# Performance work log

Measured on AMD Instinct MI355X. Metric: run time of the kernel, lower is better.

The kernel has to match this reference:

```python
import jax, jax.numpy as jnp
import numpy as np
from jax import lax

EPS = 1e-9
DN = ('NCHW', 'OIHW', 'NCHW')


def _conv2d_valid(x, w):
    return lax.conv_general_dilated(x, w, window_strides=(1, 1), padding='VALID',
                                    dimension_numbers=DN)


def setup_inputs() -> dict:
    key = jax.random.key(0)
    kx, ky = jax.random.split(key)
    x = jax.random.normal(kx, (32, 64, 96, 96), dtype=jnp.float32)
    y = jax.random.normal(ky, (32, 64, 13, 13), dtype=jnp.float32)  # (K prototypes, C, kh, kw)
    return {'x': x, 'y': y}


def reference(x, y):
    # Per-prototype L2 normalization of y over (C, kh, kw)
    y_norm = jnp.clip(jnp.sqrt(jnp.sum(y * y, axis=(1, 2, 3), keepdims=True)), EPS)
    normed_y = y / y_norm
    # Sliding-window L2 norm of x. The torch code convolves x^2 with ones of
    # shape (K, C, kh, kw) producing K identical channels; we compute one
    # channel and broadcast (same math, less work).
    ones_k = jnp.ones((1,) + y.shape[1:], dtype=x.dtype)
    x_norm = jnp.clip(jnp.sqrt(_conv2d_valid(x * x, ones_k)), EPS)  # (B,1,H',W')
    diss = _conv2d_valid(x, normed_y) / x_norm  # (B,K,H',W')
    return jax.nn.relu(diss)
```

## Files before the change

kernel.cpp:

```cpp
#include <hip/hip_runtime.h>
#include <hip/hip_bf16.h>

#define B_   32
#define C_   64
#define H_   96
#define W_   96
#define K_   32
#define R_   13
#define HO_  84
#define WO_  84
#define HW_  (H_*W_)
#define OHW_ (HO_*WO_)
#define CRR_ (C_*R_*R_)
#define RR_  (R_*R_)

#define TILE_ 16
#define PW_   28
#define NPIX_ (PW_*PW_)
#define HBUF_ 12544
#define BUF_  (2*HBUF_)
#define LDS_NEW (2*BUF_)
#define REGB_ (NPIX_*16)
#define LDS_FB (2*REGB_)

#define XBF_BYTES  ((size_t)B_*4*HW_*32)
#define UG_BYTES   ((size_t)RR_*4096)
#define S_BYTES    ((size_t)B_*HW_*4)
#define INV_BYTES  ((size_t)B_*OHW_*4)
#define WS_NEED    (XBF_BYTES + UG_BYTES + S_BYTES + INV_BYTES)

typedef unsigned int u32;
typedef unsigned short u16;
typedef __attribute__((ext_vector_type(16))) float f32x16;
typedef __attribute__((ext_vector_type(4))) u32 u32x4;

static __device__ __forceinline__ u16 f2bf(float v){
    __hip_bfloat16 h = __float2bfloat16(v);
    return *reinterpret_cast<u16*>(&h);
}

#define MFMA(acc, a, b) asm("v_mfma_f32_32x32x16_bf16 %0, %1, %2, %0" \
                            : "+v"(acc) : "v"(a), "v"(b))

static __device__ __forceinline__ void gload_lds16(const void* g, void* l){
    __builtin_amdgcn_global_load_lds(
        (const __attribute__((address_space(1))) unsigned char*)g,
        (__attribute__((address_space(3))) unsigned char*)l, 16, 0, 0);
}

static __device__ void prep_y_block(const float* __restrict__ y,
                                    unsigned char* __restrict__ u_g,
                                    int k, int tid, float* red){
    const float* yk = y + (size_t)k * CRR_;
    float ss = 0.f;
    for (int idx = tid; idx < CRR_; idx += 256){ float v = yk[idx]; ss += v*v; }
    for (int off = 32; off; off >>= 1) ss += __shfl_down(ss, off);
    if ((tid & 63) == 0) red[tid >> 6] = ss;
    __syncthreads();
    float inv = 1.f / fmaxf(sqrtf(red[0]+red[1]+red[2]+red[3]), 1e-9f);

    int c = tid & 63, grp = tid >> 6;
    int inoff = (k << 5) | ((c & 15) << 1);
    for (int base = 0; base < RR_; base += 4){
        int ij = base + grp;
        if (ij < RR_){
            int i = ij / R_, jx = ij % R_;
            float v = yk[c*RR_ + ij] * inv;
            size_t slice = ((size_t)(c >> 4) * RR_ + jx*R_ + i) << 10;
            *(u16*)(u_g + slice + inoff) = f2bf(v);
        }
    }
}

__global__ void k_prep_y(const float* __restrict__ y, unsigned char* __restrict__ u_g){
    __shared__ float red[4];
    prep_y_block(y, u_g, blockIdx.x, threadIdx.x, red);
}

__global__ void k_prep(const float* __restrict__ x, const float* __restrict__ y,
                       float* __restrict__ s, unsigned char* __restrict__ xbf,
                       unsigned char* __restrict__ u_g){
    __shared__ float red[4];
    int bb = blockIdx.x;
    if (bb < K_){ prep_y_block(y, u_g, bb, threadIdx.x, red); return; }
    int idx = (bb - K_)*256 + threadIdx.x;
    int b = idx / HW_, r = idx % HW_;
    const float* xb = x + (size_t)b * C_ * HW_ + r;
    float acc = 0.f;
    #pragma unroll
    for (int q = 0; q < 4; ++q){
        int c0 = q*16;
        float a0 = xb[(size_t)(c0+0)*HW_],  a1 = xb[(size_t)(c0+1)*HW_];
        float a2 = xb[(size_t)(c0+2)*HW_],  a3 = xb[(size_t)(c0+3)*HW_];
        float a4 = xb[(size_t)(c0+4)*HW_],  a5 = xb[(size_t)(c0+5)*HW_];
        float a6 = xb[(size_t)(c0+6)*HW_],  a7 = xb[(size_t)(c0+7)*HW_];
        float a8 = xb[(size_t)(c0+8)*HW_],  a9 = xb[(size_t)(c0+9)*HW_];
        float aa = xb[(size_t)(c0+10)*HW_], ab = xb[(size_t)(c0+11)*HW_];
        float ac = xb[(size_t)(c0+12)*HW_], ad = xb[(size_t)(c0+13)*HW_];
        float ae = xb[(size_t)(c0+14)*HW_], af = xb[(size_t)(c0+15)*HW_];
        acc += a0*a0+a1*a1+a2*a2+a3*a3+a4*a4+a5*a5+a6*a6+a7*a7
             + a8*a8+a9*a9+aa*aa+ab*ab+ac*ac+ad*ad+ae*ae+af*af;
        u32x4 q0 = { f2bf(a0)|((u32)f2bf(a1)<<16), f2bf(a2)|((u32)f2bf(a3)<<16),
                     f2bf(a4)|((u32)f2bf(a5)<<16), f2bf(a6)|((u32)f2bf(a7)<<16) };
        u32x4 q1 = { f2bf(a8)|((u32)f2bf(a9)<<16), f2bf(aa)|((u32)f2bf(ab)<<16),
                     f2bf(ac)|((u32)f2bf(ad)<<16), f2bf(ae)|((u32)f2bf(af)<<16) };
        unsigned char* ob = xbf + ((size_t)(b*4 + q)*HW_ + r)*32;
        *(u32x4*)(ob)      = q0;
        *(u32x4*)(ob + 16) = q1;
    }
    s[idx] = acc;
}

__global__ void k_sq(const float* __restrict__ x, float* __restrict__ s){
    int idx = blockIdx.x*256 + threadIdx.x;
    int b = idx / HW_, r = idx % HW_;
    const float* xb = x + (size_t)b * C_ * HW_;
    float acc = 0.f;
    #pragma unroll
    for (int c = 0; c < C_; ++c){ float v = xb[(size_t)c*HW_ + r]; acc += v*v; }
    s[idx] = acc;
}

__global__ void k_inv(const float* __restrict__ s, float* __restrict__ inv_xn){
    int idx = blockIdx.x*256 + threadIdx.x;
    int b = idx / OHW_, r = idx % OHW_;
    int oh = r / WO_, ow = r % WO_;
    const float* sb = s + (size_t)b*HW_ + oh*W_ + ow;
    float acc = 0.f;
    for (int i = 0; i < R_; ++i){
        #pragma unroll
        for (int j = 0; j < R_; ++j) acc += sb[i*W_ + j];
    }
    inv_xn[idx] = 1.f / fmaxf(sqrtf(acc), 1e-9f);
}

__launch_bounds__(256, 3)
__global__ void k_main(const unsigned char* __restrict__ xbf,
                       const unsigned char* __restrict__ u_g,
                       const float* __restrict__ inv_xn, float* __restrict__ out){
    extern __shared__ unsigned char lds[];

    int bb0 = blockIdx.x;
    int bb  = (bb0 & 7) * 144 + (bb0 >> 3);
    int b  = bb / 36;
    int tt = bb % 36;
    int oy = (tt / 6) * TILE_;
    int ox = (tt % 6) * TILE_;

    int tid  = threadIdx.x;
    int lane = tid & 63;
    int wv   = tid >> 6;
    int ks   = lane >> 5;
    int rb   = (lane >> 4) & 1;
    int cx   = lane & 15;
    int kpr  = lane & 31;

    const unsigned char* xq = xbf + (size_t)b*4*HW_*32;
    int aoff = (kpr << 5) + (ks << 4);
    int pb   = (4*wv + rb) * PW_ + cx;

    int goff[13], loff[13];
    #pragma unroll
    for (int cb = 0; cb < 13; ++cb){
        int cs = cb*64; if (cs > NPIX_-64) cs = NPIX_-64;
        int p = cs + lane;
        int py = p / PW_, px = p % PW_;
        int gy = oy + py; if (gy > H_-1) gy = H_-1;
        int gx = ox + px; if (gx > W_-1) gx = W_-1;
        goff[cb] = (gy*W_ + gx) << 5;
        loff[cb] = cs << 4;
    }

#define STAGE(bufsel, q) {                                                   \
        const unsigned char* src = xq + (size_t)(q)*HW_*32;                  \
        unsigned char* dst = lds + (bufsel)*BUF_;                            \
        for (int t = wv; t < 26; t += 4){                                    \
            int h = t & 1, cb = t >> 1;                                      \
            gload_lds16(src + goff[cb] + h*16, dst + h*HBUF_ + loff[cb]);    \
        }                                                                    \
    }

    f32x16 acc0 = {}, acc1 = {};
    STAGE(0, 0);

    for (int pass = 0; pass < 4; ++pass){
        __syncthreads();
        if (pass < 3) STAGE((pass+1)&1, pass+1);

        const unsigned char* xh = lds + (pass&1)*BUF_ + ks*HBUF_;
        const unsigned char* ug = u_g + ((size_t)pass*RR_ << 10);

        u32x4 A0 = *(const u32x4*)(ug              + aoff);
        u32x4 A1 = *(const u32x4*)(ug + (1 << 10)  + aoff);
        u32x4 A2 = *(const u32x4*)(ug + (2 << 10)  + aoff);
        u32x4 A3 = *(const u32x4*)(ug + (3 << 10)  + aoff);

        const unsigned char* col0 = xh + pb*16;
        u32x4 d0 = *(const u32x4*)(col0);
        u32x4 d1 = *(const u32x4*)(col0 +   PW_*16);
        u32x4 d2 = *(const u32x4*)(col0 + 2*PW_*16);
        u32x4 d3 = *(const u32x4*)(col0 + 3*PW_*16);
        u32x4 d4 = *(const u32x4*)(col0 + 4*PW_*16);

        int t = 0;
        for (int jx = 0; jx < R_; ++jx){
            const unsigned char* col  = xh + (pb + jx)*16;
            const unsigned char* ncol = col + 16;
            u32x4 e0, e1, e2, e3, e4;
            bool more = (jx < R_-1);
            #pragma unroll
            for (int i = 0; i < R_; ++i, ++t){
                int tn = t + 4; if (tn > RR_-1) tn = RR_-1;
                u32x4 An = *(const u32x4*)(ug + ((size_t)tn << 10) + aoff);
                u32x4 dn = d4;
                if (i < 10) dn = *(const u32x4*)(col + (i+5)*PW_*16);
                if (more){
                    if (i == 8)  e0 = *(const u32x4*)(ncol);
                    if (i == 9)  e1 = *(const u32x4*)(ncol +   PW_*16);
                    if (i == 10) e2 = *(const u32x4*)(ncol + 2*PW_*16);
                    if (i == 11) e3 = *(const u32x4*)(ncol + 3*PW_*16);
                    if (i == 12) e4 = *(const u32x4*)(ncol + 4*PW_*16);
                }
                __builtin_amdgcn_s_setprio(1);
                MFMA(acc0, A0, d0);
                MFMA(acc1, A0, d2);
                __builtin_amdgcn_s_setprio(0);
                A0 = A1; A1 = A2; A2 = A3; A3 = An;
                d0 = d1; d1 = d2; d2 = d3; d3 = d4; d4 = dn;
            }
            if (more){ d0 = e0; d1 = e1; d2 = e2; d3 = e3; d4 = e4; }
        }
    }

    int ow = ox + cx;
#define EPI(ACC, F) {                                                        \
        int oh = oy + 4*wv + rb + 2*(F);                                     \
        bool valid = (oh < HO_) && (ow < WO_);                               \
        float inv = 0.f;                                                     \
        if (valid) inv = inv_xn[(size_t)b*OHW_ + oh*WO_ + ow];               \
        float* ob = out + (size_t)b*K_*OHW_ + oh*WO_ + ow;                   \
        _Pragma("unroll")                                                    \
        for (int r = 0; r < 16; ++r){                                        \
            int kp = (r & 3) + 8*(r >> 2) + 4*ks;                            \
            if (valid) ob[(size_t)kp*OHW_] = fmaxf(ACC[r], 0.f) * inv;       \
        }                                                                    \
    }
    EPI(acc0, 0); EPI(acc1, 1);
#undef EPI
}

__launch_bounds__(256, 4)
__global__ void k_main_fb(const float* __restrict__ x, const unsigned char* __restrict__ u_g,
                          const float* __restrict__ inv_xn, float* __restrict__ out){
    extern __shared__ unsigned char lds[];
    int bb = blockIdx.x;
    int b  = bb / 36;
    int tt = bb % 36;
    int oy = (tt / 6) * TILE_;
    int ox = (tt % 6) * TILE_;
    int tid  = threadIdx.x;
    int lane = tid & 63;
    int wv   = tid >> 6;
    int ks   = lane >> 5;
    int rb   = (lane >> 4) & 1;
    int cx   = lane & 15;
    int kpr  = lane & 31;
    const float* xb = x + (size_t)b * C_ * HW_;
    int aoff = (kpr << 5) + (ks << 4);
    int pb   = (4*wv + rb) * PW_ + cx;
    f32x16 acc0 = {}, acc1 = {};
    for (int pass = 0; pass < 4; ++pass){
        if (pass) __syncthreads();
        int cbase = pass << 4;
        for (int p = tid; p < NPIX_; p += 256){
            int py = p / PW_, px = p % PW_;
            int gy = oy + py; if (gy > H_-1) gy = H_-1;
            int gx = ox + px; if (gx > W_-1) gx = W_-1;
            const float* src = xb + (size_t)cbase*HW_ + gy*W_ + gx;
            u32 w0 = f2bf(src[0*HW_])  | ((u32)f2bf(src[1*HW_])  << 16);
            u32 w1 = f2bf(src[2*HW_])  | ((u32)f2bf(src[3*HW_])  << 16);
            u32 w2 = f2bf(src[4*HW_])  | ((u32)f2bf(src[5*HW_])  << 16);
            u32 w3 = f2bf(src[6*HW_])  | ((u32)f2bf(src[7*HW_])  << 16);
            u32x4 q0 = {w0, w1, w2, w3};
            u32 v0 = f2bf(src[8*HW_])  | ((u32)f2bf(src[9*HW_])  << 16);
            u32 v1 = f2bf(src[10*HW_]) | ((u32)f2bf(src[11*HW_]) << 16);
            u32 v2 = f2bf(src[12*HW_]) | ((u32)f2bf(src[13*HW_]) << 16);
            u32 v3 = f2bf(src[14*HW_]) | ((u32)f2bf(src[15*HW_]) << 16);
            u32x4 q1 = {v0, v1, v2, v3};
            *(u32x4*)(lds +         p*16) = q0;
            *(u32x4*)(lds + REGB_ + p*16) = q1;
        }
        __syncthreads();
        const unsigned char* xh = lds + ks*REGB_;
        const unsigned char* ug = u_g + ((size_t)pass*RR_ << 10);
        u32x4 A0 = *(const u32x4*)(ug              + aoff);
        u32x4 A1 = *(const u32x4*)(ug + (1 << 10)  + aoff);
        u32x4 A2 = *(const u32x4*)(ug + (2 << 10)  + aoff);
        u32x4 A3 = *(const u32x4*)(ug + (3 << 10)  + aoff);
        int t = 0;
        for (int jx = 0; jx < R_; ++jx){
            const unsigned char* col = xh + (pb + jx)*16;
            u32x4 d0 = *(const u32x4*)(col);
            u32x4 d1 = *(const u32x4*)(col +   PW_*16);
            u32x4 d2 = *(const u32x4*)(col + 2*PW_*16);
            u32x4 d3 = *(const u32x4*)(col + 3*PW_*16);
            u32x4 d4 = *(const u32x4*)(col + 4*PW_*16);
            #pragma unroll
            for (int i = 0; i < R_; ++i, ++t){
                int tn = t + 4; if (tn > RR_-1) tn = RR_-1;
                u32x4 An = *(const u32x4*)(ug + ((size_t)tn << 10) + aoff);
                u32x4 dn = d4;
                if (i < 10) dn = *(const u32x4*)(col + (i+5)*PW_*16);
                MFMA(acc0, A0, d0);
                MFMA(acc1, A0, d2);
                A0 = A1; A1 = A2; A2 = A3; A3 = An;
                d0 = d1; d1 = d2; d2 = d3; d3 = d4; d4 = dn;
            }
        }
    }
    int ow = ox + cx;
#define EPI(ACC, F) {                                                        \
        int oh = oy + 4*wv + rb + 2*(F);                                     \
        bool valid = (oh < HO_) && (ow < WO_);                               \
        float inv = 0.f;                                                     \
        if (valid) inv = inv_xn[(size_t)b*OHW_ + oh*WO_ + ow];               \
        float* ob = out + (size_t)b*K_*OHW_ + oh*WO_ + ow;                   \
        _Pragma("unroll")                                                    \
        for (int r = 0; r < 16; ++r){                                        \
            int kp = (r & 3) + 8*(r >> 2) + 4*ks;                            \
            if (valid) ob[(size_t)kp*OHW_] = fmaxf(ACC[r], 0.f) * inv;       \
        }                                                                    \
    }
    EPI(acc0, 0); EPI(acc1, 1);
#undef EPI
}

extern "C" void kernel_launch(void* const* d_in, const int* in_sizes, int n_in,
                              void* d_out, int out_size, void* d_ws, size_t ws_size,
                              hipStream_t stream) {
    const float* x = (const float*)d_in[0];
    const float* y = (const float*)d_in[1];
    float* out = (float*)d_out;
    unsigned char* ws = (unsigned char*)d_ws;

    if (ws_size >= WS_NEED){
        unsigned char* xbf   = ws;
        unsigned char* u_g   = ws + XBF_BYTES;
        float*         s     = (float*)(ws + XBF_BYTES + UG_BYTES);
        float*         invxn = (float*)(ws + XBF_BYTES + UG_BYTES + S_BYTES);

        k_prep<<<K_ + (B_*HW_)/256, 256, 0, stream>>>(x, y, s, xbf, u_g);
        k_inv<<<(B_*OHW_)/256, 256, 0, stream>>>(s, invxn);
        k_main<<<B_*36, 256, LDS_NEW, stream>>>(xbf, u_g, invxn, out);
    } else {
        unsigned char* u_g   = ws;
        float*         s     = (float*)(ws + UG_BYTES);
        float*         invxn = (float*)(ws + UG_BYTES + S_BYTES);

        k_prep_y<<<K_, 256, 0, stream>>>(y, u_g);
        k_sq<<<(B_*HW_)/256, 256, 0, stream>>>(x, s);
        k_inv<<<(B_*OHW_)/256, 256, 0, stream>>>(s, invxn);
        k_main_fb<<<B_*36, 256, LDS_FB, stream>>>(x, u_g, invxn, out);
    }
}
```

Before: 225.6 us.

## Stage x tiles through registers into a single LDS buffer

```diff
diff --git a/kernel.cpp b/kernel.cpp
--- a/kernel.cpp
+++ b/kernel.cpp
@@ -19,7 +19,8 @@
 #define NPIX_ (PW_*PW_)
 #define HBUF_ 12544
 #define BUF_  (2*HBUF_)
-#define LDS_NEW (2*BUF_)
+#define LDS_NEW BUF_
+#define NEL_  (2*NPIX_)
 #define REGB_ (NPIX_*16)
 #define LDS_FB (2*REGB_)
 
@@ -41,12 +42,7 @@
 
 #define MFMA(acc, a, b) asm("v_mfma_f32_32x32x16_bf16 %0, %1, %2, %0" \
                             : "+v"(acc) : "v"(a), "v"(b))
-
-static __device__ __forceinline__ void gload_lds16(const void* g, void* l){
-    __builtin_amdgcn_global_load_lds(
-        (const __attribute__((address_space(1))) unsigned char*)g,
-        (__attribute__((address_space(3))) unsigned char*)l, 16, 0, 0);
-}
+#define PIN(x) asm volatile("" : "+v"(x))
 
 static __device__ void prep_y_block(const float* __restrict__ y,
                                     unsigned char* __restrict__ u_g,
@@ -159,35 +155,49 @@
     int aoff = (kpr << 5) + (ks << 4);
     int pb   = (4*wv + rb) * PW_ + cx;
 
-    int goff[13], loff[13];
+    int ge[7], le[7];
     #pragma unroll
-    for (int cb = 0; cb < 13; ++cb){
-        int cs = cb*64; if (cs > NPIX_-64) cs = NPIX_-64;
-        int p = cs + lane;
+    for (int j = 0; j < 7; ++j){
+        int e = tid + 256*j; if (e > NEL_-1) e = NEL_-1;
+        int h = (e >= NPIX_);
+        int p = e - (h ? NPIX_ : 0);
         int py = p / PW_, px = p % PW_;
         int gy = oy + py; if (gy > H_-1) gy = H_-1;
         int gx = ox + px; if (gx > W_-1) gx = W_-1;
-        goff[cb] = (gy*W_ + gx) << 5;
-        loff[cb] = cs << 4;
-    }
-
-#define STAGE(bufsel, q) {                                                   \
+        ge[j] = ((gy*W_ + gx) << 5) + h*16;
+        le[j] = p*16 + h*HBUF_;
+    }
+
+    u32x4 s0, s1, s2, s3, s4, s5, s6;
+#define LOADSTG(q) {                                                         \
         const unsigned char* src = xq + (size_t)(q)*HW_*32;                  \
-        unsigned char* dst = lds + (bufsel)*BUF_;                            \
-        for (int t = wv; t < 26; t += 4){                                    \
-            int h = t & 1, cb = t >> 1;                                      \
-            gload_lds16(src + goff[cb] + h*16, dst + h*HBUF_ + loff[cb]);    \
-        }                                                                    \
+        s0 = *(const u32x4*)(src + ge[0]); PIN(s0);                          \
+        s1 = *(const u32x4*)(src + ge[1]); PIN(s1);                          \
+        s2 = *(const u32x4*)(src + ge[2]); PIN(s2);                          \
+        s3 = *(const u32x4*)(src + ge[3]); PIN(s3);                          \
+        s4 = *(const u32x4*)(src + ge[4]); PIN(s4);                          \
+        s5 = *(const u32x4*)(src + ge[5]); PIN(s5);                          \
+        if (tid < 32){ s6 = *(const u32x4*)(src + ge[6]); PIN(s6); }         \
+    }
+#define STAGEW() {                                                           \
+        *(u32x4*)(lds + le[0]) = s0;                                         \
+        *(u32x4*)(lds + le[1]) = s1;                                         \
+        *(u32x4*)(lds + le[2]) = s2;                                         \
+        *(u32x4*)(lds + le[3]) = s3;                                         \
+        *(u32x4*)(lds + le[4]) = s4;                                         \
+        *(u32x4*)(lds + le[5]) = s5;                                         \
+        if (tid < 32) *(u32x4*)(lds + le[6]) = s6;                           \
     }
 
     f32x16 acc0 = {}, acc1 = {};
-    STAGE(0, 0);
+    LOADSTG(0);
+    STAGEW();
+    __syncthreads();
 
     for (int pass = 0; pass < 4; ++pass){
-        __syncthreads();
-        if (pass < 3) STAGE((pass+1)&1, pass+1);
-
-        const unsigned char* xh = lds + (pass&1)*BUF_ + ks*HBUF_;
+        if (pass < 3) LOADSTG(pass+1);
+
+        const unsigned char* xh = lds + ks*HBUF_;
         const unsigned char* ug = u_g + ((size_t)pass*RR_ << 10);
 
         u32x4 A0 = *(const u32x4*)(ug              + aoff);
@@ -207,20 +217,18 @@
             const unsigned char* col  = xh + (pb + jx)*16;
             const unsigned char* ncol = col + 16;
             u32x4 e0, e1, e2, e3, e4;
-            bool more = (jx < R_-1);
             #pragma unroll
             for (int i = 0; i < R_; ++i, ++t){
                 int tn = t + 4; if (tn > RR_-1) tn = RR_-1;
                 u32x4 An = *(const u32x4*)(ug + ((size_t)tn << 10) + aoff);
                 u32x4 dn = d4;
                 if (i < 10) dn = *(const u32x4*)(col + (i+5)*PW_*16);
-                if (more){
-                    if (i == 8)  e0 = *(const u32x4*)(ncol);
-                    if (i == 9)  e1 = *(const u32x4*)(ncol +   PW_*16);
-                    if (i == 10) e2 = *(const u32x4*)(ncol + 2*PW_*16);
-                    if (i == 11) e3 = *(const u32x4*)(ncol + 3*PW_*16);
-                    if (i == 12) e4 = *(const u32x4*)(ncol + 4*PW_*16);
-                }
+                PIN(dn);
+                if (i == 8){  e0 = *(const u32x4*)(ncol);             PIN(e0); }
+                if (i == 9){  e1 = *(const u32x4*)(ncol +   PW_*16);  PIN(e1); }
+                if (i == 10){ e2 = *(const u32x4*)(ncol + 2*PW_*16);  PIN(e2); }
+                if (i == 11){ e3 = *(const u32x4*)(ncol + 3*PW_*16);  PIN(e3); }
+                if (i == 12){ e4 = *(const u32x4*)(ncol + 4*PW_*16);  PIN(e4); }
                 __builtin_amdgcn_s_setprio(1);
                 MFMA(acc0, A0, d0);
                 MFMA(acc1, A0, d2);
@@ -228,7 +236,13 @@
                 A0 = A1; A1 = A2; A2 = A3; A3 = An;
                 d0 = d1; d1 = d2; d2 = d3; d3 = d4; d4 = dn;
             }
-            if (more){ d0 = e0; d1 = e1; d2 = e2; d3 = e3; d4 = e4; }
+            d0 = e0; d1 = e1; d2 = e2; d3 = e3; d4 = e4;
+        }
+
+        if (pass < 3){
+            __syncthreads();
+            STAGEW();
+            __syncthreads();
         }
     }
 
```

New measurement: 244.2 us. +8.2%, slower.

## Enlarge k_main output tile to 24 rows with three accumulators per wave

Applied to the files above, without the earlier changes.

```diff
diff --git a/kernel.cpp b/kernel.cpp
--- a/kernel.cpp
+++ b/kernel.cpp
@@ -16,10 +16,14 @@
 
 #define TILE_ 16
 #define PW_   28
+#define TLV_  24
+#define PH_   36
+#define NPIX2_ (PH_*PW_)
+#define NEL2_  (2*NPIX2_)
+#define HB2_   (NPIX2_*16)
+#define BUF2_  (2*HB2_)
+#define LDS2_  (2*BUF2_)
 #define NPIX_ (PW_*PW_)
-#define HBUF_ 12544
-#define BUF_  (2*HBUF_)
-#define LDS_NEW (2*BUF_)
 #define REGB_ (NPIX_*16)
 #define LDS_FB (2*REGB_)
 
@@ -134,17 +138,17 @@
     inv_xn[idx] = 1.f / fmaxf(sqrtf(acc), 1e-9f);
 }
 
-__launch_bounds__(256, 3)
+__launch_bounds__(256, 2)
 __global__ void k_main(const unsigned char* __restrict__ xbf,
                        const unsigned char* __restrict__ u_g,
                        const float* __restrict__ inv_xn, float* __restrict__ out){
     extern __shared__ unsigned char lds[];
 
     int bb0 = blockIdx.x;
-    int bb  = (bb0 & 7) * 144 + (bb0 >> 3);
-    int b  = bb / 36;
-    int tt = bb % 36;
-    int oy = (tt / 6) * TILE_;
+    int bb  = (bb0 & 7) * 96 + (bb0 >> 3);
+    int b  = bb / 24;
+    int tt = bb % 24;
+    int oy = (tt / 6) * TLV_;
     int ox = (tt % 6) * TILE_;
 
     int tid  = threadIdx.x;
@@ -157,37 +161,39 @@
 
     const unsigned char* xq = xbf + (size_t)b*4*HW_*32;
     int aoff = (kpr << 5) + (ks << 4);
-    int pb   = (4*wv + rb) * PW_ + cx;
-
-    int goff[13], loff[13];
+    int pb   = (6*wv + rb) * PW_ + cx;
+
+    int goff[8], loff[8];
     #pragma unroll
-    for (int cb = 0; cb < 13; ++cb){
-        int cs = cb*64; if (cs > NPIX_-64) cs = NPIX_-64;
-        int p = cs + lane;
+    for (int j = 0; j < 8; ++j){
+        int cb = wv + 4*j;
+        int cs = cb*64; if (cs > NEL2_-64) cs = NEL2_-64;
+        int e = cs + lane;
+        int h = (e >= NPIX2_);
+        int p = e - (h ? NPIX2_ : 0);
         int py = p / PW_, px = p % PW_;
         int gy = oy + py; if (gy > H_-1) gy = H_-1;
         int gx = ox + px; if (gx > W_-1) gx = W_-1;
-        goff[cb] = (gy*W_ + gx) << 5;
-        loff[cb] = cs << 4;
+        goff[j] = ((gy*W_ + gx) << 5) + h*16;
+        loff[j] = cs << 4;
     }
 
 #define STAGE(bufsel, q) {                                                   \
         const unsigned char* src = xq + (size_t)(q)*HW_*32;                  \
-        unsigned char* dst = lds + (bufsel)*BUF_;                            \
-        for (int t = wv; t < 26; t += 4){                                    \
-            int h = t & 1, cb = t >> 1;                                      \
-            gload_lds16(src + goff[cb] + h*16, dst + h*HBUF_ + loff[cb]);    \
-        }                                                                    \
-    }
-
-    f32x16 acc0 = {}, acc1 = {};
+        unsigned char* dst = lds + (bufsel)*BUF2_;                           \
+        _Pragma("unroll")                                                    \
+        for (int j = 0; j < 8; ++j)                                          \
+            gload_lds16(src + goff[j], dst + loff[j]);                       \
+    }
+
+    f32x16 acc0 = {}, acc1 = {}, acc2 = {};
     STAGE(0, 0);
 
     for (int pass = 0; pass < 4; ++pass){
         __syncthreads();
         if (pass < 3) STAGE((pass+1)&1, pass+1);
 
-        const unsigned char* xh = lds + (pass&1)*BUF_ + ks*HBUF_;
+        const unsigned char* xh = lds + (pass&1)*BUF2_ + ks*HB2_;
         const unsigned char* ug = u_g + ((size_t)pass*RR_ << 10);
 
         u32x4 A0 = *(const u32x4*)(ug              + aoff);
@@ -196,45 +202,45 @@
         u32x4 A3 = *(const u32x4*)(ug + (3 << 10)  + aoff);
 
         const unsigned char* col0 = xh + pb*16;
-        u32x4 d0 = *(const u32x4*)(col0);
-        u32x4 d1 = *(const u32x4*)(col0 +   PW_*16);
-        u32x4 d2 = *(const u32x4*)(col0 + 2*PW_*16);
-        u32x4 d3 = *(const u32x4*)(col0 + 3*PW_*16);
-        u32x4 d4 = *(const u32x4*)(col0 + 4*PW_*16);
+        u32x4 w0 = *(const u32x4*)(col0);
+        u32x4 w1 = *(const u32x4*)(col0 +   PW_*16);
+        u32x4 w2 = *(const u32x4*)(col0 + 2*PW_*16);
+        u32x4 w3 = *(const u32x4*)(col0 + 3*PW_*16);
+        u32x4 w4 = *(const u32x4*)(col0 + 4*PW_*16);
+        u32x4 w5 = *(const u32x4*)(col0 + 5*PW_*16);
 
         int t = 0;
         for (int jx = 0; jx < R_; ++jx){
             const unsigned char* col  = xh + (pb + jx)*16;
             const unsigned char* ncol = col + 16;
-            u32x4 e0, e1, e2, e3, e4;
-            bool more = (jx < R_-1);
+            u32x4 e0, e1, e2, e3, e4, e5;
             #pragma unroll
             for (int i = 0; i < R_; ++i, ++t){
                 int tn = t + 4; if (tn > RR_-1) tn = RR_-1;
                 u32x4 An = *(const u32x4*)(ug + ((size_t)tn << 10) + aoff);
-                u32x4 dn = d4;
-                if (i < 10) dn = *(const u32x4*)(col + (i+5)*PW_*16);
-                if (more){
-                    if (i == 8)  e0 = *(const u32x4*)(ncol);
-                    if (i == 9)  e1 = *(const u32x4*)(ncol +   PW_*16);
-                    if (i == 10) e2 = *(const u32x4*)(ncol + 2*PW_*16);
-                    if (i == 11) e3 = *(const u32x4*)(ncol + 3*PW_*16);
-                    if (i == 12) e4 = *(const u32x4*)(ncol + 4*PW_*16);
-                }
+                u32x4 wn = w5;
+                if (i < 11) wn = *(const u32x4*)(col + (i+6)*PW_*16);
+                if (i == 7)  e0 = *(const u32x4*)(ncol);
+                if (i == 8)  e1 = *(const u32x4*)(ncol +   PW_*16);
+                if (i == 9)  e2 = *(const u32x4*)(ncol + 2*PW_*16);
+                if (i == 10) e3 = *(const u32x4*)(ncol + 3*PW_*16);
+                if (i == 11) e4 = *(const u32x4*)(ncol + 4*PW_*16);
+                if (i == 12) e5 = *(const u32x4*)(ncol + 5*PW_*16);
                 __builtin_amdgcn_s_setprio(1);
-                MFMA(acc0, A0, d0);
-                MFMA(acc1, A0, d2);
+                MFMA(acc0, A0, w0);
+                MFMA(acc1, A0, w2);
+                MFMA(acc2, A0, w4);
                 __builtin_amdgcn_s_setprio(0);
                 A0 = A1; A1 = A2; A2 = A3; A3 = An;
-                d0 = d1; d1 = d2; d2 = d3; d3 = d4; d4 = dn;
+                w0 = w1; w1 = w2; w2 = w3; w3 = w4; w4 = w5; w5 = wn;
             }
-            if (more){ d0 = e0; d1 = e1; d2 = e2; d3 = e3; d4 = e4; }
+            w0 = e0; w1 = e1; w2 = e2; w3 = e3; w4 = e4; w5 = e5;
         }
     }
 
     int ow = ox + cx;
 #define EPI(ACC, F) {                                                        \
-        int oh = oy + 4*wv + rb + 2*(F);                                     \
+        int oh = oy + 6*wv + rb + 2*(F);                                     \
         bool valid = (oh < HO_) && (ow < WO_);                               \
         float inv = 0.f;                                                     \
         if (valid) inv = inv_xn[(size_t)b*OHW_ + oh*WO_ + ow];               \
@@ -245,7 +251,7 @@
             if (valid) ob[(size_t)kp*OHW_] = fmaxf(ACC[r], 0.f) * inv;       \
         }                                                                    \
     }
-    EPI(acc0, 0); EPI(acc1, 1);
+    EPI(acc0, 0); EPI(acc1, 1); EPI(acc2, 2);
 #undef EPI
 }
 
@@ -351,7 +357,7 @@
 
         k_prep<<<K_ + (B_*HW_)/256, 256, 0, stream>>>(x, y, s, xbf, u_g);
         k_inv<<<(B_*OHW_)/256, 256, 0, stream>>>(s, invxn);
-        k_main<<<B_*36, 256, LDS_NEW, stream>>>(xbf, u_g, invxn, out);
+        k_main<<<B_*24, 256, LDS2_, stream>>>(xbf, u_g, invxn, out);
     } else {
         unsigned char* u_g   = ws;
         float*         s     = (float*)(ws + UG_BYTES);
```

After: 199.8 us. 1.13x faster.
